# Kernel tuning notes

Hardware: AMD Instinct MI355X
Metric: run time of the kernel (lower is better)

## Reference

```python
import jax, jax.numpy as jnp
import numpy as np

EPS = 1e-9


def setup_inputs() -> dict:
    key = jax.random.key(0)
    kE, kQ, kK, kV = jax.random.split(key, 4)
    B, S, D = 8, 2048, 256
    return {
        "E": jax.random.normal(kE, (B, S, D), dtype=jnp.float32),
        "WQ": jax.random.normal(kQ, (D, D), dtype=jnp.float32) * (1.0 / np.sqrt(D)),
        "WK": jax.random.normal(kK, (D, D), dtype=jnp.float32) * (1.0 / np.sqrt(D)),
        "WV": jax.random.normal(kV, (D, D), dtype=jnp.float32) * (1.0 / np.sqrt(D)),
    }


def reference(E, WQ, WK, WV):
    # E: [B, S, D]; WQ/WK/WV: [D, D] (torch Linear weight, applied as x @ W.T)
    D = E.shape[-1]
    scale = jnp.asarray(np.sqrt(D), dtype=E.dtype)
    Q = jnp.einsum('bsd,ed->bse', E, WQ)
    K = jnp.einsum('bsd,ed->bse', E, WK)
    V = jnp.einsum('bsd,ed->bse', E, WV)
    # Full score matrix [B, S, S] (non-flash, as in the original)
    W = jnp.einsum('bqd,bkd->bqk', Q, K) / scale
    # mask=True path: causal tril mask, additionally zeroed where W == 0 exactly
    S_len = W.shape[-1]
    tril = jnp.tril(jnp.ones((S_len, S_len), dtype=W.dtype))  # [S, S]
    M = jnp.where(W == 0, jnp.zeros_like(W), tril[None, :, :])
    # custom masked softmax with epsilon denominator
    x_max = jnp.max(W, axis=-1, keepdims=True)
    x_exp = jnp.exp(W - x_max) * M
    A = x_exp / (jnp.sum(x_exp, axis=-1, keepdims=True) + EPS)
    return jnp.einsum('bqk,bkd->bqd', A, V)
```

## Files before the change

kernel.cpp:

```cpp
#include <hip/hip_runtime.h>
#include <hip/hip_bf16.h>
#include <stdint.h>


typedef __attribute__((ext_vector_type(8)))  short bf16x8;
typedef __attribute__((ext_vector_type(4)))  float f32x4;
typedef __attribute__((ext_vector_type(16))) float f32x16;
typedef __attribute__((ext_vector_type(4)))  unsigned int u32x4;

#define NEGF  -3.0e38f
#define MINIT -1.0e30f

__device__ __forceinline__ unsigned short f2bf(float f){
  union { float f; unsigned u; } v; v.f = f;
  unsigned r = v.u + 0x7FFFu + ((v.u >> 16) & 1u);
  return (unsigned short)(r >> 16);
}
__device__ __forceinline__ unsigned pk2(float a, float b){
  return (unsigned)f2bf(a) | ((unsigned)f2bf(b) << 16);
}
__device__ __forceinline__ unsigned short f2bf_n(float f){
  __hip_bfloat16 h = __float2bfloat16(f);
  return *reinterpret_cast<unsigned short*>(&h);
}
__device__ __forceinline__ unsigned pk2_n(float a, float b){
  return (unsigned)f2bf_n(a) | ((unsigned)f2bf_n(b) << 16);
}
__device__ __forceinline__ float bf2f(unsigned short h){
  union { unsigned u; float f; } v; v.u = ((unsigned)h) << 16; return v.f;
}

__device__ __host__ __forceinline__ int nch_of(int tau, int sched){
  return (sched == 2 && tau >= 20) ? 4 : 2;
}
__device__ __forceinline__ int pbase_of(int tau, int sched){
  if (sched == 2) return (tau <= 20) ? tau : 20 + (tau - 20)*3;
  return tau;
}
__device__ __forceinline__ int mlbase_of(int tau, int sched){
  if (sched == 2) return (tau <= 20) ? 2*tau : 40 + (tau - 20)*4;
  return 2*tau;
}

__global__ void wconv_kernel(const float* __restrict__ WQ, const float* __restrict__ WK,
                             const float* __restrict__ WV, unsigned short* __restrict__ Wb)
{
  const int widx = blockIdx.x, kk = blockIdx.y, n = threadIdx.x;
  const float* W = (widx==0) ? WQ : ((widx==1) ? WK : WV);
  unsigned short* dst = Wb + (size_t)widx*65536 + kk*8192 + n*32;
#pragma unroll
  for (int gp=0; gp<4; ++gp){
    const int g = gp ^ (n & 3);
    const float* src = W + (size_t)n*256 + kk*32 + g*8;
    float4 a = *reinterpret_cast<const float4*>(src);
    float4 c = *reinterpret_cast<const float4*>(src + 4);
    uint4 v; v.x = pk2(a.x,a.y); v.y = pk2(a.z,a.w); v.z = pk2(c.x,c.y); v.w = pk2(c.z,c.w);
    *reinterpret_cast<uint4*>(dst + gp*8) = v;
  }
}

__global__ __launch_bounds__(256, 3) void qkv_proj_kernel(
    const float* __restrict__ E, const unsigned short* __restrict__ Wb,
    unsigned short* __restrict__ Qb, unsigned short* __restrict__ Ka,
    unsigned short* __restrict__ Vf)
{
  __shared__ unsigned short As[32*256];
  __shared__ unsigned short Bs[2][8192];

  const int m0 = blockIdx.x * 32;
  const int b  = m0 >> 11;
  const int sb = m0 & 2047;
  const int t = threadIdx.x, lane = t & 63, w = t >> 6;
  const int hi = lane >> 4, lo = lane & 15;

  auto stageB = [&](int widx, int kk, int buf){
    const char* src = (const char*)Wb + widx*131072 + kk*16384;
    char* dst = (char*)Bs[buf];
#pragma unroll
    for (int c=0;c<4;c++){
      const int off = c*4096 + t*16;
      __builtin_amdgcn_global_load_lds(
        (const __attribute__((address_space(1))) unsigned int*)(src + off),
        (__attribute__((address_space(3))) unsigned int*)(dst + off), 16, 0, 0);
    }
  };

  stageB(0, 0, 0);
  {
    const int r = t >> 3, c0 = (t & 7) * 32;
    const float* ga = E + (size_t)(m0 + r)*256 + c0;
#pragma unroll
    for (int gg=0; gg<4; ++gg){
      float4 x = *reinterpret_cast<const float4*>(ga + gg*8);
      float4 y = *reinterpret_cast<const float4*>(ga + gg*8 + 4);
      uint4 v; v.x = pk2(x.x,x.y); v.y = pk2(x.z,x.w); v.z = pk2(y.x,y.y); v.w = pk2(y.z,y.w);
      const int g = (t & 7)*4 + gg;
      *reinterpret_cast<uint4*>((char*)As + r*512 + ((g ^ (r & 7)) << 4)) = v;
    }
  }

  const f32x4 fzero = {0.f,0.f,0.f,0.f};
  const int u = sb >> 5;
  for (int widx=0; widx<3; ++widx){
    f32x4 acc[2][4];
#pragma unroll
    for (int mi=0;mi<2;mi++)
#pragma unroll
      for (int f=0;f<4;f++) acc[mi][f] = fzero;
    if (widx) stageB(widx, 0, 0);

    for (int kk=0; kk<8; ++kk){
      const int bb = kk & 1;
      if (kk < 7) stageB(widx, kk+1, bb^1);
      if (kk < 7) asm volatile("s_waitcnt vmcnt(4) lgkmcnt(0)" ::: "memory");
      else        asm volatile("s_waitcnt vmcnt(0) lgkmcnt(0)" ::: "memory");
      __builtin_amdgcn_sched_barrier(0);
      __builtin_amdgcn_s_barrier();
      __builtin_amdgcn_sched_barrier(0);

      bf16x8 afr[2], bfr[4];
#pragma unroll
      for (int mi=0;mi<2;mi++){
        const int r = mi*16 + lo;
        afr[mi] = *reinterpret_cast<const bf16x8*>(
            (const char*)As + r*512 + (((kk*4 + hi) ^ (r & 7)) << 4));
      }
#pragma unroll
      for (int f=0;f<4;f++){
        const int n = w*64 + f*16 + lo;
        bfr[f] = *reinterpret_cast<const bf16x8*>(
            (const char*)Bs[bb] + n*64 + ((hi ^ (n & 3)) << 4));
      }
#pragma unroll
      for (int mi=0;mi<2;mi++)
#pragma unroll
        for (int f=0;f<4;f++)
          acc[mi][f] = __builtin_amdgcn_mfma_f32_16x16x32_bf16(afr[mi], bfr[f], acc[mi][f], 0,0,0);

      asm volatile("s_waitcnt lgkmcnt(0)" ::: "memory");
      __builtin_amdgcn_sched_barrier(0);
      __builtin_amdgcn_s_barrier();
    }

    if (widx == 0){
#pragma unroll
      for (int mi=0;mi<2;mi++)
#pragma unroll
        for (int f=0;f<4;f++){
          const int col = w*64 + f*16 + lo;
#pragma unroll
          for (int r=0;r<4;r++)
            Qb[(size_t)(m0 + mi*16 + hi*4 + r)*256 + col] = f2bf(acc[mi][f][r]*0.0625f);
        }
    } else if (widx == 1){
      unsigned short* Kab = Ka + (size_t)b*524288 + (size_t)u*8192;
#pragma unroll
      for (int mi=0;mi<2;mi++)
#pragma unroll
        for (int f=0;f<4;f++){
          const int c = w*4 + f;
          const int j = lo & 7;
          const int lb = 32*(lo>>3) + mi*16 + hi*4;
#pragma unroll
          for (int r=0;r<4;r++)
            Kab[(size_t)(c*64 + lb + r)*8 + j] = f2bf(acc[mi][f][r]);
        }
    } else {
      unsigned short* Vfb = Vf + (size_t)b*524288;
#pragma unroll
      for (int mi=0;mi<2;mi++)
#pragma unroll
        for (int f=0;f<4;f++){
          const int d  = w*64 + f*16 + lo;
          const int dt = d >> 5;
          const int l  = 32*(hi&1) + (d&31);
          const int j0 = 4*(hi>>1);
          unsigned short* vp = Vfb + ((size_t)((u*2 + mi)*8 + dt)*64 + l)*8 + j0;
          uint2 pw; pw.x = pk2(acc[mi][f][0], acc[mi][f][1]);
          pw.y = pk2(acc[mi][f][2], acc[mi][f][3]);
          *reinterpret_cast<uint2*>(vp) = pw;
        }
    }
  }
}

__global__ __launch_bounds__(256, 2) void attn_kernel(
    const unsigned short* __restrict__ Qb, const unsigned short* __restrict__ Ka,
    const unsigned short* __restrict__ Vf, float* __restrict__ Out,
    const int sched, unsigned short* __restrict__ Pb, float* __restrict__ ML,
    const int psl, const int mls)
{
  __shared__ char Lds[2][32768];

  const int bid  = blockIdx.x;
  const int b    = bid & 7;
  const int slot = bid >> 3;
  int tau, chunk, mode, u0, u1;
  if (sched == 2){
    int nch;
    if (slot < 8)       { tau = 19 - (slot >> 1); chunk = slot & 1;      nch = 2; }
    else if (slot < 56) { int s = slot - 8;  tau = 31 - (s >> 2); chunk = s & 3; nch = 4; }
    else                { int s = slot - 56; tau = 15 - (s >> 1); chunk = s & 1; nch = 2; }
    const int len = 2*tau + 2;
    const int qq = len / nch, rem = len - qq*nch;
    u0 = chunk*qq + ((chunk < rem) ? chunk : rem);
    u1 = u0 + qq + ((chunk < rem) ? 1 : 0);
    mode = (chunk == 0) ? 1 : 2;
  } else if (sched == 1){
    const int ts = slot >> 1; chunk = slot & 1;
    tau = (ts < 16) ? (31 - ts) : (ts - 16);
    u0 = chunk ? (tau + 1) : 0;
    u1 = chunk ? (2*tau + 2) : (tau + 1);
    mode = 1 + chunk;
  } else {
    tau = 31 - slot; chunk = 0; u0 = 0; u1 = 2*tau + 2; mode = 0;
  }
  const int Qbase = tau * 64;

  const int t = threadIdx.x;
  const int lane = t & 63, w = t >> 6;
  const int qs = w >> 1, dh = w & 1;
  const int l31 = lane & 31, h5 = lane >> 5;
  const int q_l = Qbase + qs*32 + l31;
  const int diagu = 2*tau + qs;

  const char* Kab = (const char*)Ka + (size_t)b*1048576;
  const char* Vfb = (const char*)Vf + (size_t)b*1048576;

  auto stage = [&](int uu, int buf){
    const char* gk = Kab + (size_t)uu*16384;
    const char* gv = Vfb + (size_t)uu*16384;
    char* lk = Lds[buf];
    char* lv = Lds[buf] + 16384;
#pragma unroll
    for (int i=0;i<4;i++){
      const int off = i*4096 + t*16;
      __builtin_amdgcn_global_load_lds(
        (const __attribute__((address_space(1))) unsigned int*)(gk + off),
        (__attribute__((address_space(3))) unsigned int*)(lk + off), 16, 0, 0);
      __builtin_amdgcn_global_load_lds(
        (const __attribute__((address_space(1))) unsigned int*)(gv + off),
        (__attribute__((address_space(3))) unsigned int*)(lv + off), 16, 0, 0);
    }
  };

  bf16x8 qf[16];
  {
    const unsigned short* Qp = Qb + ((size_t)(b*2048 + q_l))*256 + h5*8;
#pragma unroll
    for (int c=0;c<16;c++) qf[c] = *reinterpret_cast<const bf16x8*>(Qp + c*16);
  }

  const f32x16 z16 = {0.f,0.f,0.f,0.f,0.f,0.f,0.f,0.f,0.f,0.f,0.f,0.f,0.f,0.f,0.f,0.f};
  f32x16 accO[4];
#pragma unroll
  for (int i=0;i<4;i++) accO[i] = z16;
  float m_run = MINIT, l_run = 0.f;

  stage(u0, 0);
  if (u0 + 1 < u1) stage(u0 + 1, 1);

  for (int u = u0; u < u1; ++u){
    const int buf = (u - u0) & 1;
    if (u + 1 < u1) asm volatile("s_waitcnt vmcnt(8)" ::: "memory");
    else            asm volatile("s_waitcnt vmcnt(0)" ::: "memory");
    __builtin_amdgcn_sched_barrier(0);
    __builtin_amdgcn_s_barrier();
    __builtin_amdgcn_sched_barrier(0);

    const char* kt = Lds[buf];
    const char* lv = Lds[buf] + 16384 + dh*4096 + lane*16;

    f32x16 sv0 = z16, sv1 = z16, sv2 = z16, sv3 = z16;
#pragma unroll
    for (int c=0;c<16;c+=4){
      bf16x8 a0 = *reinterpret_cast<const bf16x8*>(kt + c*1024 + lane*16);
      bf16x8 a1 = *reinterpret_cast<const bf16x8*>(kt + (c+1)*1024 + lane*16);
      bf16x8 a2 = *reinterpret_cast<const bf16x8*>(kt + (c+2)*1024 + lane*16);
      bf16x8 a3 = *reinterpret_cast<const bf16x8*>(kt + (c+3)*1024 + lane*16);
      sv0 = __builtin_amdgcn_mfma_f32_32x32x16_bf16(a0, qf[c],   sv0, 0,0,0);
      sv1 = __builtin_amdgcn_mfma_f32_32x32x16_bf16(a1, qf[c+1], sv1, 0,0,0);
      sv2 = __builtin_amdgcn_mfma_f32_32x32x16_bf16(a2, qf[c+2], sv2, 0,0,0);
      sv3 = __builtin_amdgcn_mfma_f32_32x32x16_bf16(a3, qf[c+3], sv3, 0,0,0);
    }
    f32x16 s16 = (sv0 + sv1) + (sv2 + sv3);

    bf16x8 vf0[4], vf1[4];
#pragma unroll
    for (int i=0;i<4;i++){
      vf0[i] = *reinterpret_cast<const bf16x8*>(lv + i*1024);
      vf1[i] = *reinterpret_cast<const bf16x8*>(lv + 8192 + i*1024);
    }

    if (u >= diagu){
      const int kvb = u*32 + 4*h5;
#pragma unroll
      for (int r=0;r<16;r++){
        const int kv = kvb + (r&3) + 8*(r>>2);
        if (kv > q_l) s16[r] = NEGF;
      }
    }

    float t8[8], t4[4];
#pragma unroll
    for (int i=0;i<8;i++) t8[i] = fmaxf(s16[i], s16[i+8]);
#pragma unroll
    for (int i=0;i<4;i++) t4[i] = fmaxf(t8[i], t8[i+4]);
    float pmax = fmaxf(fmaxf(t4[0],t4[1]), fmaxf(t4[2],t4[3]));
    pmax = fmaxf(pmax, __shfl_xor(pmax, 32, 64));

    if (!__all(pmax - m_run <= 8.0f)){
      const float mn = fmaxf(m_run, pmax);
      const float alpha = __expf(m_run - mn);
#pragma unroll
      for (int i=0;i<4;i++) accO[i] *= alpha;
      l_run *= alpha;
      m_run = mn;
    }
    float p[16];
#pragma unroll
    for (int r=0;r<16;r++) p[r] = __expf(s16[r] - m_run);
#pragma unroll
    for (int i=0;i<8;i++) t8[i] = p[i] + p[i+8];
#pragma unroll
    for (int i=0;i<4;i++) t4[i] = t8[i] + t8[i+4];
    float ls = (t4[0]+t4[1]) + (t4[2]+t4[3]);
    ls += __shfl_xor(ls, 32, 64);
    l_run += ls;

    union { bf16x8 v; unsigned u32[4]; } pa0, pa1;
#pragma unroll
    for (int k=0;k<4;k++){
      pa0.u32[k] = pk2_n(p[2*k],   p[2*k+1]);
      pa1.u32[k] = pk2_n(p[8+2*k], p[9+2*k]);
    }

#pragma unroll
    for (int i=0;i<4;i++){
      accO[i] = __builtin_amdgcn_mfma_f32_32x32x16_bf16(vf0[i], pa0.v, accO[i], 0,0,0);
      accO[i] = __builtin_amdgcn_mfma_f32_32x32x16_bf16(vf1[i], pa1.v, accO[i], 0,0,0);
    }

    asm volatile("s_waitcnt lgkmcnt(0)" ::: "memory");
    __builtin_amdgcn_sched_barrier(0);
    __builtin_amdgcn_s_barrier();
    if (u + 2 < u1) stage(u + 2, buf);
  }

  if (mode && dh == 0 && lane < 32){
    float* mlp = ML + ((size_t)(b*mls + mlbase_of(tau, sched) + chunk)*64 + qs*32 + lane)*2;
    mlp[0] = m_run; mlp[1] = l_run;
  }

  const float inv = (mode == 0) ? 1.0f/(l_run + 1e-9f) : 1.0f;
  float* Tw = (float*)(&Lds[0][0]) + w*2048;
  const int qloc = lane >> 1, dc = (lane & 1) * 16;
#pragma unroll
  for (int i=0;i<4;i++){
#pragma unroll
    for (int r=0;r<16;r++)
      Tw[l31*33 + ((r&3) + 8*(r>>2) + 4*h5)] = accO[i][r] * inv;
    asm volatile("s_waitcnt lgkmcnt(0)" ::: "memory");
    __builtin_amdgcn_sched_barrier(0);
    const float* srcT = &Tw[qloc*33 + dc];
    if (mode < 2){
      float* dst = Out + ((size_t)(b*2048 + Qbase + qs*32 + qloc))*256 + dh*128 + i*32 + dc;
#pragma unroll
      for (int k=0;k<4;k++){
        float4 vv = { srcT[4*k], srcT[4*k+1], srcT[4*k+2], srcT[4*k+3] };
        *reinterpret_cast<float4*>(dst + 4*k) = vv;
      }
    } else {
      unsigned short* pb = Pb + ((size_t)(b*psl + pbase_of(tau, sched) + (chunk-1))*64 + qs*32 + qloc)*256
                              + dh*128 + i*32 + dc;
      u32x4 w0, w1;
      w0.x = pk2_n(srcT[0],  srcT[1]);  w0.y = pk2_n(srcT[2],  srcT[3]);
      w0.z = pk2_n(srcT[4],  srcT[5]);  w0.w = pk2_n(srcT[6],  srcT[7]);
      w1.x = pk2_n(srcT[8],  srcT[9]);  w1.y = pk2_n(srcT[10], srcT[11]);
      w1.z = pk2_n(srcT[12], srcT[13]); w1.w = pk2_n(srcT[14], srcT[15]);
      *reinterpret_cast<u32x4*>(pb)     = w0;
      *reinterpret_cast<u32x4*>(pb + 8) = w1;
    }
    asm volatile("s_waitcnt lgkmcnt(0)" ::: "memory");
    __builtin_amdgcn_sched_barrier(0);
  }
}

__global__ void combine_kernel(float* __restrict__ Out, const unsigned short* __restrict__ Pb,
                               const float* __restrict__ ML, const int sched,
                               const int psl, const int mls)
{
  const int b = blockIdx.x & 7, tt = blockIdx.x >> 3;
  const int nch = nch_of(tt, sched);
  const int pbase = (sched == 2) ? ((tt <= 20) ? tt : 20 + (tt - 20)*3) : tt;
  const int mlbase = (sched == 2) ? ((tt <= 20) ? 2*tt : 40 + (tt - 20)*4) : 2*tt;
  const int t = threadIdx.x;
  const int q = t >> 2, dg = (t & 3) * 64;

  float mc[4], lc[4];
#pragma unroll
  for (int c=0;c<4;c++){
    if (c < nch){
      const float* mlp = ML + ((size_t)(b*mls + mlbase + c)*64 + q)*2;
      mc[c] = mlp[0]; lc[c] = mlp[1];
    } else { mc[c] = MINIT; lc[c] = 0.f; }
  }
  float M = fmaxf(fmaxf(mc[0],mc[1]), fmaxf(mc[2],mc[3]));
  float e[4], L = 0.f;
#pragma unroll
  for (int c=0;c<4;c++){ e[c] = __expf(mc[c] - M); L += e[c]*lc[c]; }
  const float inv = 1.0f/(L + 1e-9f);

  float* O = Out + ((size_t)(b*2048 + tt*64 + q))*256 + dg;
  f32x4 acc[16];
#pragma unroll
  for (int k=0;k<16;k++){
    f32x4 v = *reinterpret_cast<const f32x4*>(O + 4*k);
    acc[k] = v * e[0];
  }
#pragma unroll
  for (int c=1;c<4;c++){
    if (c < nch){
      const unsigned short* P = Pb + ((size_t)(b*psl + pbase + (c-1))*64 + q)*256 + dg;
#pragma unroll
      for (int k=0;k<8;k++){
        u32x4 pv = *reinterpret_cast<const u32x4*>(P + 8*k);
        const unsigned short* us = (const unsigned short*)&pv;
#pragma unroll
        for (int j=0;j<4;j++) acc[2*k][j]   += e[c]*bf2f(us[j]);
#pragma unroll
        for (int j=0;j<4;j++) acc[2*k+1][j] += e[c]*bf2f(us[4+j]);
      }
    }
  }
#pragma unroll
  for (int k=0;k<16;k++){
    f32x4 v = acc[k] * inv;
    *reinterpret_cast<f32x4*>(O + 4*k) = v;
  }
}

extern "C" void kernel_launch(void* const* d_in, const int* in_sizes, int n_in,
                              void* d_out, int out_size, void* d_ws, size_t ws_size,
                              hipStream_t stream)
{
  const float* E  = (const float*)d_in[0];
  const float* WQ = (const float*)d_in[1];
  const float* WK = (const float*)d_in[2];
  const float* WV = (const float*)d_in[3];
  const size_t elems = (size_t)8*2048*256;

  unsigned short* Qb = (unsigned short*)d_ws;
  unsigned short* Ka = Qb + elems;
  unsigned short* Vf = Ka + elems;
  unsigned short* Wb = Vf + elems;
  const size_t base = 3*elems*2 + 393216;

  const size_t PB2 = (size_t)8*56*64*256*2, ML2 = (size_t)8*88*64*2*4;
  const size_t PB1 = (size_t)8*32*64*256*2, ML1 = (size_t)8*64*64*2*4;
  if (ws_size < base) return;
  int sched = 0, psl = 0, mls = 0, grid = 256;
  if (ws_size >= base + PB2 + ML2){ sched = 2; psl = 56; mls = 88; grid = 704; }
  else if (ws_size >= base + PB1 + ML1){ sched = 1; psl = 32; mls = 64; grid = 512; }
  unsigned short* Pb = (unsigned short*)((char*)d_ws + base);
  float* ML = (float*)((char*)d_ws + base + ((sched == 2) ? PB2 : PB1));

  wconv_kernel<<<dim3(3,8), 256, 0, stream>>>(WQ, WK, WV, Wb);
  qkv_proj_kernel<<<512, 256, 0, stream>>>(E, Wb, Qb, Ka, Vf);
  attn_kernel<<<grid, 256, 0, stream>>>(Qb, Ka, Vf, (float*)d_out, sched, Pb, ML, psl, mls);
  if (sched) combine_kernel<<<256, 256, 0, stream>>>((float*)d_out, Pb, ML, sched, psl, mls);
}
```

Baseline: 92.03 us.

## Replace static attention split schedule with persistent atomic work queue

```diff
diff --git a/kernel.cpp b/kernel.cpp
--- a/kernel.cpp
+++ b/kernel.cpp
@@ -11,14 +11,6 @@
 #define NEGF  -3.0e38f
 #define MINIT -1.0e30f
 
-__device__ __forceinline__ unsigned short f2bf(float f){
-  union { float f; unsigned u; } v; v.f = f;
-  unsigned r = v.u + 0x7FFFu + ((v.u >> 16) & 1u);
-  return (unsigned short)(r >> 16);
-}
-__device__ __forceinline__ unsigned pk2(float a, float b){
-  return (unsigned)f2bf(a) | ((unsigned)f2bf(b) << 16);
-}
 __device__ __forceinline__ unsigned short f2bf_n(float f){
   __hip_bfloat16 h = __float2bfloat16(f);
   return *reinterpret_cast<unsigned short*>(&h);
@@ -30,22 +22,12 @@
   union { unsigned u; float f; } v; v.u = ((unsigned)h) << 16; return v.f;
 }
 
-__device__ __host__ __forceinline__ int nch_of(int tau, int sched){
-  return (sched == 2 && tau >= 20) ? 4 : 2;
-}
-__device__ __forceinline__ int pbase_of(int tau, int sched){
-  if (sched == 2) return (tau <= 20) ? tau : 20 + (tau - 20)*3;
-  return tau;
-}
-__device__ __forceinline__ int mlbase_of(int tau, int sched){
-  if (sched == 2) return (tau <= 20) ? 2*tau : 40 + (tau - 20)*4;
-  return 2*tau;
-}
-
 __global__ void wconv_kernel(const float* __restrict__ WQ, const float* __restrict__ WK,
-                             const float* __restrict__ WV, unsigned short* __restrict__ Wb)
+                             const float* __restrict__ WV, unsigned short* __restrict__ Wb,
+                             int* __restrict__ Qctr)
 {
   const int widx = blockIdx.x, kk = blockIdx.y, n = threadIdx.x;
+  if (Qctr && widx == 0 && kk == 0 && n < 8) Qctr[n] = 0;
   const float* W = (widx==0) ? WQ : ((widx==1) ? WK : WV);
   unsigned short* dst = Wb + (size_t)widx*65536 + kk*8192 + n*32;
 #pragma unroll
@@ -54,7 +36,7 @@
     const float* src = W + (size_t)n*256 + kk*32 + g*8;
     float4 a = *reinterpret_cast<const float4*>(src);
     float4 c = *reinterpret_cast<const float4*>(src + 4);
-    uint4 v; v.x = pk2(a.x,a.y); v.y = pk2(a.z,a.w); v.z = pk2(c.x,c.y); v.w = pk2(c.z,c.w);
+    uint4 v; v.x = pk2_n(a.x,a.y); v.y = pk2_n(a.z,a.w); v.z = pk2_n(c.x,c.y); v.w = pk2_n(c.z,c.w);
     *reinterpret_cast<uint4*>(dst + gp*8) = v;
   }
 }
@@ -93,7 +75,7 @@
     for (int gg=0; gg<4; ++gg){
       float4 x = *reinterpret_cast<const float4*>(ga + gg*8);
       float4 y = *reinterpret_cast<const float4*>(ga + gg*8 + 4);
-      uint4 v; v.x = pk2(x.x,x.y); v.y = pk2(x.z,x.w); v.z = pk2(y.x,y.y); v.w = pk2(y.z,y.w);
+      uint4 v; v.x = pk2_n(x.x,x.y); v.y = pk2_n(x.z,x.w); v.z = pk2_n(y.x,y.y); v.w = pk2_n(y.z,y.w);
       const int g = (t & 7)*4 + gg;
       *reinterpret_cast<uint4*>((char*)As + r*512 + ((g ^ (r & 7)) << 4)) = v;
     }
@@ -150,7 +132,7 @@
           const int col = w*64 + f*16 + lo;
 #pragma unroll
           for (int r=0;r<4;r++)
-            Qb[(size_t)(m0 + mi*16 + hi*4 + r)*256 + col] = f2bf(acc[mi][f][r]*0.0625f);
+            Qb[(size_t)(m0 + mi*16 + hi*4 + r)*256 + col] = f2bf_n(acc[mi][f][r]*0.0625f);
         }
     } else if (widx == 1){
       unsigned short* Kab = Ka + (size_t)b*524288 + (size_t)u*8192;
@@ -163,7 +145,7 @@
           const int lb = 32*(lo>>3) + mi*16 + hi*4;
 #pragma unroll
           for (int r=0;r<4;r++)
-            Kab[(size_t)(c*64 + lb + r)*8 + j] = f2bf(acc[mi][f][r]);
+            Kab[(size_t)(c*64 + lb + r)*8 + j] = f2bf_n(acc[mi][f][r]);
         }
     } else {
       unsigned short* Vfb = Vf + (size_t)b*524288;
@@ -176,8 +158,8 @@
           const int l  = 32*(hi&1) + (d&31);
           const int j0 = 4*(hi>>1);
           unsigned short* vp = Vfb + ((size_t)((u*2 + mi)*8 + dt)*64 + l)*8 + j0;
-          uint2 pw; pw.x = pk2(acc[mi][f][0], acc[mi][f][1]);
-          pw.y = pk2(acc[mi][f][2], acc[mi][f][3]);
+          uint2 pw; pw.x = pk2_n(acc[mi][f][0], acc[mi][f][1]);
+          pw.y = pk2_n(acc[mi][f][2], acc[mi][f][3]);
           *reinterpret_cast<uint2*>(vp) = pw;
         }
     }
@@ -188,41 +170,17 @@
     const unsigned short* __restrict__ Qb, const unsigned short* __restrict__ Ka,
     const unsigned short* __restrict__ Vf, float* __restrict__ Out,
     const int sched, unsigned short* __restrict__ Pb, float* __restrict__ ML,
-    const int psl, const int mls)
+    int* __restrict__ Qctr)
 {
   __shared__ char Lds[2][32768];
+  __shared__ int s_slot;
 
   const int bid  = blockIdx.x;
   const int b    = bid & 7;
-  const int slot = bid >> 3;
-  int tau, chunk, mode, u0, u1;
-  if (sched == 2){
-    int nch;
-    if (slot < 8)       { tau = 19 - (slot >> 1); chunk = slot & 1;      nch = 2; }
-    else if (slot < 56) { int s = slot - 8;  tau = 31 - (s >> 2); chunk = s & 3; nch = 4; }
-    else                { int s = slot - 56; tau = 15 - (s >> 1); chunk = s & 1; nch = 2; }
-    const int len = 2*tau + 2;
-    const int qq = len / nch, rem = len - qq*nch;
-    u0 = chunk*qq + ((chunk < rem) ? chunk : rem);
-    u1 = u0 + qq + ((chunk < rem) ? 1 : 0);
-    mode = (chunk == 0) ? 1 : 2;
-  } else if (sched == 1){
-    const int ts = slot >> 1; chunk = slot & 1;
-    tau = (ts < 16) ? (31 - ts) : (ts - 16);
-    u0 = chunk ? (tau + 1) : 0;
-    u1 = chunk ? (2*tau + 2) : (tau + 1);
-    mode = 1 + chunk;
-  } else {
-    tau = 31 - slot; chunk = 0; u0 = 0; u1 = 2*tau + 2; mode = 0;
-  }
-  const int Qbase = tau * 64;
-
   const int t = threadIdx.x;
   const int lane = t & 63, w = t >> 6;
   const int qs = w >> 1, dh = w & 1;
   const int l31 = lane & 31, h5 = lane >> 5;
-  const int q_l = Qbase + qs*32 + l31;
-  const int diagu = 2*tau + qs;
 
   const char* Kab = (const char*)Ka + (size_t)b*1048576;
   const char* Vfb = (const char*)Vf + (size_t)b*1048576;
@@ -244,156 +202,191 @@
     }
   };
 
-  bf16x8 qf[16];
-  {
-    const unsigned short* Qp = Qb + ((size_t)(b*2048 + q_l))*256 + h5*8;
-#pragma unroll
-    for (int c=0;c<16;c++) qf[c] = *reinterpret_cast<const bf16x8*>(Qp + c*16);
-  }
-
   const f32x16 z16 = {0.f,0.f,0.f,0.f,0.f,0.f,0.f,0.f,0.f,0.f,0.f,0.f,0.f,0.f,0.f,0.f};
-  f32x16 accO[4];
-#pragma unroll
-  for (int i=0;i<4;i++) accO[i] = z16;
-  float m_run = MINIT, l_run = 0.f;
-
-  stage(u0, 0);
-  if (u0 + 1 < u1) stage(u0 + 1, 1);
-
-  for (int u = u0; u < u1; ++u){
-    const int buf = (u - u0) & 1;
-    if (u + 1 < u1) asm volatile("s_waitcnt vmcnt(8)" ::: "memory");
-    else            asm volatile("s_waitcnt vmcnt(0)" ::: "memory");
-    __builtin_amdgcn_sched_barrier(0);
-    __builtin_amdgcn_s_barrier();
-    __builtin_amdgcn_sched_barrier(0);
-
-    const char* kt = Lds[buf];
-    const char* lv = Lds[buf] + 16384 + dh*4096 + lane*16;
-
-    f32x16 sv0 = z16, sv1 = z16, sv2 = z16, sv3 = z16;
-#pragma unroll
-    for (int c=0;c<16;c+=4){
-      bf16x8 a0 = *reinterpret_cast<const bf16x8*>(kt + c*1024 + lane*16);
-      bf16x8 a1 = *reinterpret_cast<const bf16x8*>(kt + (c+1)*1024 + lane*16);
-      bf16x8 a2 = *reinterpret_cast<const bf16x8*>(kt + (c+2)*1024 + lane*16);
-      bf16x8 a3 = *reinterpret_cast<const bf16x8*>(kt + (c+3)*1024 + lane*16);
-      sv0 = __builtin_amdgcn_mfma_f32_32x32x16_bf16(a0, qf[c],   sv0, 0,0,0);
-      sv1 = __builtin_amdgcn_mfma_f32_32x32x16_bf16(a1, qf[c+1], sv1, 0,0,0);
-      sv2 = __builtin_amdgcn_mfma_f32_32x32x16_bf16(a2, qf[c+2], sv2, 0,0,0);
-      sv3 = __builtin_amdgcn_mfma_f32_32x32x16_bf16(a3, qf[c+3], sv3, 0,0,0);
-    }
-    f32x16 s16 = (sv0 + sv1) + (sv2 + sv3);
-
-    bf16x8 vf0[4], vf1[4];
+
+  for (;;){
+    int slot;
+    if (sched == 2){
+      __syncthreads();
+      if (t == 0) s_slot = atomicAdd(&Qctr[b], 1);
+      __syncthreads();
+      slot = s_slot;
+      if (slot >= 128) break;
+    } else {
+      slot = bid >> 3;
+    }
+
+    int tau, chunk, mode, u0, u1;
+    if (sched == 2){
+      tau = 31 - (slot >> 2); chunk = slot & 3;
+      const int len = 2*tau + 2, qq = len >> 2, rem = len & 3;
+      u0 = chunk*qq + ((chunk < rem) ? chunk : rem);
+      u1 = u0 + qq + ((chunk < rem) ? 1 : 0);
+      mode = (chunk == 0) ? 1 : 2;
+    } else if (sched == 1){
+      const int ts = slot >> 1; chunk = slot & 1;
+      tau = (ts < 16) ? (31 - ts) : (ts - 16);
+      u0 = chunk ? (tau + 1) : 0;
+      u1 = chunk ? (2*tau + 2) : (tau + 1);
+      mode = 1 + chunk;
+    } else {
+      tau = 31 - slot; chunk = 0; u0 = 0; u1 = 2*tau + 2; mode = 0;
+    }
+    const int Qbase = tau * 64;
+    const int q_l = Qbase + qs*32 + l31;
+    const int diagu = 2*tau + qs;
+
+    bf16x8 qf[16];
+    {
+      const unsigned short* Qp = Qb + ((size_t)(b*2048 + q_l))*256 + h5*8;
+#pragma unroll
+      for (int c=0;c<16;c++) qf[c] = *reinterpret_cast<const bf16x8*>(Qp + c*16);
+    }
+
+    f32x16 accO[4];
+#pragma unroll
+    for (int i=0;i<4;i++) accO[i] = z16;
+    float m_run = MINIT, l_run = 0.f;
+
+    if (u0 < u1){
+      stage(u0, 0);
+      if (u0 + 1 < u1) stage(u0 + 1, 1);
+
+      for (int u = u0; u < u1; ++u){
+        const int buf = (u - u0) & 1;
+        if (u + 1 < u1) asm volatile("s_waitcnt vmcnt(8)" ::: "memory");
+        else            asm volatile("s_waitcnt vmcnt(0)" ::: "memory");
+        __builtin_amdgcn_sched_barrier(0);
+        __builtin_amdgcn_s_barrier();
+        __builtin_amdgcn_sched_barrier(0);
+
+        const char* kt = Lds[buf];
+        const char* lv = Lds[buf] + 16384 + dh*4096 + lane*16;
+
+        f32x16 sv0 = z16, sv1 = z16;
+#pragma unroll
+        for (int c=0;c<16;c+=2){
+          bf16x8 a0 = *reinterpret_cast<const bf16x8*>(kt + c*1024 + lane*16);
+          bf16x8 a1 = *reinterpret_cast<const bf16x8*>(kt + (c+1)*1024 + lane*16);
+          sv0 = __builtin_amdgcn_mfma_f32_32x32x16_bf16(a0, qf[c],   sv0, 0,0,0);
+          sv1 = __builtin_amdgcn_mfma_f32_32x32x16_bf16(a1, qf[c+1], sv1, 0,0,0);
+        }
+        f32x16 s16 = sv0 + sv1;
+
+        bf16x8 vf0[4], vf1[4];
+#pragma unroll
+        for (int i=0;i<4;i++){
+          vf0[i] = *reinterpret_cast<const bf16x8*>(lv + i*1024);
+          vf1[i] = *reinterpret_cast<const bf16x8*>(lv + 8192 + i*1024);
+        }
+
+        if (u >= diagu){
+          const int kvb = u*32 + 4*h5;
+#pragma unroll
+          for (int r=0;r<16;r++){
+            const int kv = kvb + (r&3) + 8*(r>>2);
+            if (kv > q_l) s16[r] = NEGF;
+          }
+        }
+
+        float t8[8], t4[4];
+#pragma unroll
+        for (int i=0;i<8;i++) t8[i] = fmaxf(s16[i], s16[i+8]);
+#pragma unroll
+        for (int i=0;i<4;i++) t4[i] = fmaxf(t8[i], t8[i+4]);
+        float pmax = fmaxf(fmaxf(t4[0],t4[1]), fmaxf(t4[2],t4[3]));
+        pmax = fmaxf(pmax, __shfl_xor(pmax, 32, 64));
+
+        if (!__all(pmax - m_run <= 8.0f)){
+          const float mn = fmaxf(m_run, pmax);
+          const float alpha = __expf(m_run - mn);
+#pragma unroll
+          for (int i=0;i<4;i++) accO[i] *= alpha;
+          l_run *= alpha;
+          m_run = mn;
+        }
+        float p[16];
+#pragma unroll
+        for (int r=0;r<16;r++) p[r] = __expf(s16[r] - m_run);
+#pragma unroll
+        for (int i=0;i<8;i++) t8[i] = p[i] + p[i+8];
+#pragma unroll
+        for (int i=0;i<4;i++) t4[i] = t8[i] + t8[i+4];
+        float ls = (t4[0]+t4[1]) + (t4[2]+t4[3]);
+        ls += __shfl_xor(ls, 32, 64);
+        l_run += ls;
+
+        union { bf16x8 v; unsigned u32[4]; } pa0, pa1;
+#pragma unroll
+        for (int k=0;k<4;k++){
+          pa0.u32[k] = pk2_n(p[2*k],   p[2*k+1]);
+          pa1.u32[k] = pk2_n(p[8+2*k], p[9+2*k]);
+        }
+
+#pragma unroll
+        for (int i=0;i<4;i++){
+          accO[i] = __builtin_amdgcn_mfma_f32_32x32x16_bf16(vf0[i], pa0.v, accO[i], 0,0,0);
+          accO[i] = __builtin_amdgcn_mfma_f32_32x32x16_bf16(vf1[i], pa1.v, accO[i], 0,0,0);
+        }
+
+        asm volatile("s_waitcnt lgkmcnt(0)" ::: "memory");
+        __builtin_amdgcn_sched_barrier(0);
+        __builtin_amdgcn_s_barrier();
+        if (u + 2 < u1) stage(u + 2, buf);
+      }
+    }
+
+    if (mode && dh == 0 && lane < 32){
+      const int nch = (sched == 2) ? 4 : 2;
+      float* mlp = ML + ((size_t)(((b*32 + tau)*nch + chunk)*64 + qs*32 + lane))*2;
+      mlp[0] = m_run; mlp[1] = l_run;
+    }
+
+    __syncthreads();
+
+    const float inv = (mode == 0) ? 1.0f/(l_run + 1e-9f) : 1.0f;
+    float* Tw = (float*)(&Lds[0][0]) + w*2048;
+    const int qloc = lane >> 1, dc = (lane & 1) * 16;
 #pragma unroll
     for (int i=0;i<4;i++){
-      vf0[i] = *reinterpret_cast<const bf16x8*>(lv + i*1024);
-      vf1[i] = *reinterpret_cast<const bf16x8*>(lv + 8192 + i*1024);
-    }
-
-    if (u >= diagu){
-      const int kvb = u*32 + 4*h5;
-#pragma unroll
-      for (int r=0;r<16;r++){
-        const int kv = kvb + (r&3) + 8*(r>>2);
-        if (kv > q_l) s16[r] = NEGF;
+#pragma unroll
+      for (int r=0;r<16;r++)
+        Tw[l31*33 + ((r&3) + 8*(r>>2) + 4*h5)] = accO[i][r] * inv;
+      asm volatile("s_waitcnt lgkmcnt(0)" ::: "memory");
+      __builtin_amdgcn_sched_barrier(0);
+      const float* srcT = &Tw[qloc*33 + dc];
+      if (mode < 2){
+        float* dst = Out + ((size_t)(b*2048 + Qbase + qs*32 + qloc))*256 + dh*128 + i*32 + dc;
+#pragma unroll
+        for (int k=0;k<4;k++){
+          float4 vv = { srcT[4*k], srcT[4*k+1], srcT[4*k+2], srcT[4*k+3] };
+          *reinterpret_cast<float4*>(dst + 4*k) = vv;
+        }
+      } else {
+        const int psl = (sched == 2) ? 3 : 1;
+        unsigned short* pb = Pb + ((size_t)((b*32 + tau)*psl + (chunk-1))*64 + qs*32 + qloc)*256
+                                + dh*128 + i*32 + dc;
+        u32x4 w0, w1;
+        w0.x = pk2_n(srcT[0],  srcT[1]);  w0.y = pk2_n(srcT[2],  srcT[3]);
+        w0.z = pk2_n(srcT[4],  srcT[5]);  w0.w = pk2_n(srcT[6],  srcT[7]);
+        w1.x = pk2_n(srcT[8],  srcT[9]);  w1.y = pk2_n(srcT[10], srcT[11]);
+        w1.z = pk2_n(srcT[12], srcT[13]); w1.w = pk2_n(srcT[14], srcT[15]);
+        *reinterpret_cast<u32x4*>(pb)     = w0;
+        *reinterpret_cast<u32x4*>(pb + 8) = w1;
       }
-    }
-
-    float t8[8], t4[4];
-#pragma unroll
-    for (int i=0;i<8;i++) t8[i] = fmaxf(s16[i], s16[i+8]);
-#pragma unroll
-    for (int i=0;i<4;i++) t4[i] = fmaxf(t8[i], t8[i+4]);
-    float pmax = fmaxf(fmaxf(t4[0],t4[1]), fmaxf(t4[2],t4[3]));
-    pmax = fmaxf(pmax, __shfl_xor(pmax, 32, 64));
-
-    if (!__all(pmax - m_run <= 8.0f)){
-      const float mn = fmaxf(m_run, pmax);
-      const float alpha = __expf(m_run - mn);
-#pragma unroll
-      for (int i=0;i<4;i++) accO[i] *= alpha;
-      l_run *= alpha;
-      m_run = mn;
-    }
-    float p[16];
-#pragma unroll
-    for (int r=0;r<16;r++) p[r] = __expf(s16[r] - m_run);
-#pragma unroll
-    for (int i=0;i<8;i++) t8[i] = p[i] + p[i+8];
-#pragma unroll
-    for (int i=0;i<4;i++) t4[i] = t8[i] + t8[i+4];
-    float ls = (t4[0]+t4[1]) + (t4[2]+t4[3]);
-    ls += __shfl_xor(ls, 32, 64);
-    l_run += ls;
-
-    union { bf16x8 v; unsigned u32[4]; } pa0, pa1;
-#pragma unroll
-    for (int k=0;k<4;k++){
-      pa0.u32[k] = pk2_n(p[2*k],   p[2*k+1]);
-      pa1.u32[k] = pk2_n(p[8+2*k], p[9+2*k]);
-    }
-
-#pragma unroll
-    for (int i=0;i<4;i++){
-      accO[i] = __builtin_amdgcn_mfma_f32_32x32x16_bf16(vf0[i], pa0.v, accO[i], 0,0,0);
-      accO[i] = __builtin_amdgcn_mfma_f32_32x32x16_bf16(vf1[i], pa1.v, accO[i], 0,0,0);
-    }
-
-    asm volatile("s_waitcnt lgkmcnt(0)" ::: "memory");
-    __builtin_amdgcn_sched_barrier(0);
-    __builtin_amdgcn_s_barrier();
-    if (u + 2 < u1) stage(u + 2, buf);
-  }
-
-  if (mode && dh == 0 && lane < 32){
-    float* mlp = ML + ((size_t)(b*mls + mlbase_of(tau, sched) + chunk)*64 + qs*32 + lane)*2;
-    mlp[0] = m_run; mlp[1] = l_run;
-  }
-
-  const float inv = (mode == 0) ? 1.0f/(l_run + 1e-9f) : 1.0f;
-  float* Tw = (float*)(&Lds[0][0]) + w*2048;
-  const int qloc = lane >> 1, dc = (lane & 1) * 16;
-#pragma unroll
-  for (int i=0;i<4;i++){
-#pragma unroll
-    for (int r=0;r<16;r++)
-      Tw[l31*33 + ((r&3) + 8*(r>>2) + 4*h5)] = accO[i][r] * inv;
-    asm volatile("s_waitcnt lgkmcnt(0)" ::: "memory");
-    __builtin_amdgcn_sched_barrier(0);
-    const float* srcT = &Tw[qloc*33 + dc];
-    if (mode < 2){
-      float* dst = Out + ((size_t)(b*2048 + Qbase + qs*32 + qloc))*256 + dh*128 + i*32 + dc;
-#pragma unroll
-      for (int k=0;k<4;k++){
-        float4 vv = { srcT[4*k], srcT[4*k+1], srcT[4*k+2], srcT[4*k+3] };
-        *reinterpret_cast<float4*>(dst + 4*k) = vv;
-      }
-    } else {
-      unsigned short* pb = Pb + ((size_t)(b*psl + pbase_of(tau, sched) + (chunk-1))*64 + qs*32 + qloc)*256
-                              + dh*128 + i*32 + dc;
-      u32x4 w0, w1;
-      w0.x = pk2_n(srcT[0],  srcT[1]);  w0.y = pk2_n(srcT[2],  srcT[3]);
-      w0.z = pk2_n(srcT[4],  srcT[5]);  w0.w = pk2_n(srcT[6],  srcT[7]);
-      w1.x = pk2_n(srcT[8],  srcT[9]);  w1.y = pk2_n(srcT[10], srcT[11]);
-      w1.z = pk2_n(srcT[12], srcT[13]); w1.w = pk2_n(srcT[14], srcT[15]);
-      *reinterpret_cast<u32x4*>(pb)     = w0;
-      *reinterpret_cast<u32x4*>(pb + 8) = w1;
-    }
-    asm volatile("s_waitcnt lgkmcnt(0)" ::: "memory");
-    __builtin_amdgcn_sched_barrier(0);
+      asm volatile("s_waitcnt lgkmcnt(0)" ::: "memory");
+      __builtin_amdgcn_sched_barrier(0);
+    }
+
+    if (sched != 2) break;
   }
 }
 
 __global__ void combine_kernel(float* __restrict__ Out, const unsigned short* __restrict__ Pb,
-                               const float* __restrict__ ML, const int sched,
-                               const int psl, const int mls)
+                               const float* __restrict__ ML, const int sched)
 {
+  const int nch = (sched == 2) ? 4 : 2, psl = nch - 1;
   const int b = blockIdx.x & 7, tt = blockIdx.x >> 3;
-  const int nch = nch_of(tt, sched);
-  const int pbase = (sched == 2) ? ((tt <= 20) ? tt : 20 + (tt - 20)*3) : tt;
-  const int mlbase = (sched == 2) ? ((tt <= 20) ? 2*tt : 40 + (tt - 20)*4) : 2*tt;
   const int t = threadIdx.x;
   const int q = t >> 2, dg = (t & 3) * 64;
 
@@ -401,7 +394,7 @@
 #pragma unroll
   for (int c=0;c<4;c++){
     if (c < nch){
-      const float* mlp = ML + ((size_t)(b*mls + mlbase + c)*64 + q)*2;
+      const float* mlp = ML + ((size_t)(((b*32 + tt)*nch + c)*64 + q))*2;
       mc[c] = mlp[0]; lc[c] = mlp[1];
     } else { mc[c] = MINIT; lc[c] = 0.f; }
   }
@@ -421,7 +414,7 @@
 #pragma unroll
   for (int c=1;c<4;c++){
     if (c < nch){
-      const unsigned short* P = Pb + ((size_t)(b*psl + pbase + (c-1))*64 + q)*256 + dg;
+      const unsigned short* P = Pb + ((size_t)((b*32 + tt)*psl + (c-1))*64 + q)*256 + dg;
 #pragma unroll
       for (int k=0;k<8;k++){
         u32x4 pv = *reinterpret_cast<const u32x4*>(P + 8*k);
@@ -456,17 +449,20 @@
   unsigned short* Wb = Vf + elems;
   const size_t base = 3*elems*2 + 393216;
 
-  const size_t PB2 = (size_t)8*56*64*256*2, ML2 = (size_t)8*88*64*2*4;
-  const size_t PB1 = (size_t)8*32*64*256*2, ML1 = (size_t)8*64*64*2*4;
+  const size_t PB2 = (size_t)8*32*3*64*256*2;
+  const size_t ML2 = (size_t)8*32*4*64*2*4;
+  const size_t PB1 = (size_t)8*32*64*256*2;
+  const size_t ML1 = (size_t)8*32*2*64*2*4;
   if (ws_size < base) return;
-  int sched = 0, psl = 0, mls = 0, grid = 256;
-  if (ws_size >= base + PB2 + ML2){ sched = 2; psl = 56; mls = 88; grid = 704; }
-  else if (ws_size >= base + PB1 + ML1){ sched = 1; psl = 32; mls = 64; grid = 512; }
+  int sched = 0;
+  if      (ws_size >= base + PB2 + ML2 + 64) sched = 2;
+  else if (ws_size >= base + PB1 + ML1)      sched = 1;
   unsigned short* Pb = (unsigned short*)((char*)d_ws + base);
   float* ML = (float*)((char*)d_ws + base + ((sched == 2) ? PB2 : PB1));
-
-  wconv_kernel<<<dim3(3,8), 256, 0, stream>>>(WQ, WK, WV, Wb);
+  int* Qctr = (sched == 2) ? (int*)((char*)d_ws + base + PB2 + ML2) : (int*)0;
+
+  wconv_kernel<<<dim3(3,8), 256, 0, stream>>>(WQ, WK, WV, Wb, Qctr);
   qkv_proj_kernel<<<512, 256, 0, stream>>>(E, Wb, Qb, Ka, Vf);
-  attn_kernel<<<grid, 256, 0, stream>>>(Qb, Ka, Vf, (float*)d_out, sched, Pb, ML, psl, mls);
-  if (sched) combine_kernel<<<256, 256, 0, stream>>>((float*)d_out, Pb, ML, sched, psl, mls);
-}
+  attn_kernel<<<sched ? 512 : 256, 256, 0, stream>>>(Qb, Ka, Vf, (float*)d_out, sched, Pb, ML, Qctr);
+  if (sched) combine_kernel<<<256, 256, 0, stream>>>((float*)d_out, Pb, ML, sched);
+}
```

Result: slower. 95.84 us (+4.1%).
